# Kernel optimization log

Hardware: AMD Instinct MI355X
Metric: run time of the kernel (lower is better)

The kernel has to match this reference:

```python
import jax, jax.numpy as jnp
import numpy as np

IN_DIM, OUT_DIM, RANK = 4096, 4096, 16

def setup_inputs() -> dict:
    key = jax.random.key(0)
    k_x, k_w, k_a, k_b = jax.random.split(key, 4)
    x = jax.random.normal(k_x, (8, 2048, IN_DIM), dtype=jnp.float32)
    weight = jax.random.normal(k_w, (OUT_DIM, IN_DIM), dtype=jnp.float32)
    bias = jnp.zeros((OUT_DIM,), dtype=jnp.float32)
    # orthogonal-ish init for A, B via QR on gaussian
    A = jnp.linalg.qr(jax.random.normal(k_a, (IN_DIM, RANK), dtype=jnp.float32))[0]
    B = jnp.linalg.qr(jax.random.normal(k_b, (OUT_DIM, RANK), dtype=jnp.float32))[0].T
    return {"x": x, "A": A, "B": B, "weight": weight, "bias": bias}

def reference(x, A, B, weight, bias):
    # eval-mode dropout == identity, so
    # x @ (weight.T + A@B) + bias == x@weight.T + (x@A)@B + bias (fused low-rank path)
    base = jnp.einsum('bsd,od->bso', x, weight)
    lora = jnp.einsum('bsr,ro->bso', jnp.einsum('bsd,dr->bsr', x, A), B)
    return base + lora + bias
```

## Files before the change

### kernel.cpp

```cpp
#include <hip/hip_runtime.h>
#include <hip/hip_bf16.h>
#include <cstdint>

#define M_DIM 16384
#define K_DIM 4096
#define N_DIM 4096
#define RANK  16

#define BM 128
#define BN 128
#define BK 64

typedef __bf16 bf16x8 __attribute__((ext_vector_type(8)));
typedef float  f32x4  __attribute__((ext_vector_type(4)));

__device__ __forceinline__ uint16_t f2bf(float f) {
    union { float f; uint32_t u; } v; v.f = f;
    uint32_t u = v.u;
    return (uint16_t)((u + 0x7FFFu + ((u >> 16) & 1u)) >> 16);
}

#define CVT_BLOCKS (M_DIM * K_DIM / (8 * 256))

__global__ void prep_kernel(const float* __restrict__ x, uint16_t* __restrict__ xb,
                            const float* __restrict__ W, const float* __restrict__ A,
                            const float* __restrict__ B, uint16_t* __restrict__ wb) {
    if (blockIdx.x < CVT_BLOCKS) {
        size_t g = (size_t)blockIdx.x * blockDim.x + threadIdx.x;
        const float4* xv = (const float4*)x;
        float4 a = xv[2 * g];
        float4 b = xv[2 * g + 1];
        union { uint4 u; uint16_t h[8]; } p;
        p.h[0] = f2bf(a.x); p.h[1] = f2bf(a.y); p.h[2] = f2bf(a.z); p.h[3] = f2bf(a.w);
        p.h[4] = f2bf(b.x); p.h[5] = f2bf(b.y); p.h[6] = f2bf(b.z); p.h[7] = f2bf(b.w);
        ((uint4*)xb)[g] = p.u;
    } else {
        const int n = blockIdx.x - CVT_BLOCKS;
        __shared__ float bcol[RANK];
        if (threadIdx.x < RANK) bcol[threadIdx.x] = B[threadIdx.x * N_DIM + n];
        __syncthreads();
        float bc[RANK];
#pragma unroll
        for (int r = 0; r < RANK; r++) bc[r] = bcol[r];
        for (int k = threadIdx.x; k < K_DIM; k += blockDim.x) {
            const float4* ar = (const float4*)(A + (size_t)k * RANK);
            float acc = W[(size_t)n * K_DIM + k];
#pragma unroll
            for (int q = 0; q < 4; q++) {
                float4 a4 = ar[q];
                acc += a4.x * bc[4*q+0] + a4.y * bc[4*q+1] + a4.z * bc[4*q+2] + a4.w * bc[4*q+3];
            }
            wb[(size_t)n * K_DIM + k] = f2bf(acc);
        }
    }
}

__device__ __forceinline__ void gload_lds16(const void* g, void* l) {
    __builtin_amdgcn_global_load_lds(
        (const __attribute__((address_space(1))) void*)g,
        (__attribute__((address_space(3))) void*)l,
        16, 0, 0);
}

__global__ __launch_bounds__(256, 3)
void gemm_bt_bias(const uint16_t* __restrict__ Xb,
                  const uint16_t* __restrict__ Wb,
                  const float* __restrict__ bias,
                  float* __restrict__ C) {
    __shared__ uint16_t As[BM * BK];
    __shared__ uint16_t Bs[BN * BK];

    const int tid  = threadIdx.x;
    const int wave = tid >> 6;
    const int lane = tid & 63;

    const int bm = blockIdx.y * BM;
    const int bn = blockIdx.x * BN;

    const int wm = (wave >> 1) * 64;
    const int wn = (wave & 1) * 64;

    const uint16_t* xg[4];
    const uint16_t* wg[4];
    uint16_t* lA[4];
    uint16_t* lB[4];
#pragma unroll
    for (int s = 0; s < 4; s++) {
        const int c   = tid + 256 * s;
        const int row = c >> 3;
        const int ql  = c & 7;
        const int qg  = ql ^ (row & 7);
        xg[s] = Xb + (size_t)(bm + row) * K_DIM + qg * 8;
        wg[s] = Wb + (size_t)(bn + row) * K_DIM + qg * 8;
        lA[s] = As + c * 8;
        lB[s] = Bs + c * 8;
    }

    const int m15 = lane & 15;
    const int kq  = lane >> 4;

    int aoff[4][2], boff[4][2];
#pragma unroll
    for (int i = 0; i < 4; i++) {
        const int ra = wm + i * 16 + m15;
        const int rb = wn + i * 16 + m15;
#pragma unroll
        for (int h = 0; h < 2; h++) {
            const int kc = h * 4 + kq;
            aoff[i][h] = (ra * 8 + (kc ^ (ra & 7))) * 8;
            boff[i][h] = (rb * 8 + (kc ^ (rb & 7))) * 8;
        }
    }

    f32x4 acc[4][4];
    const f32x4 zero = {0.f, 0.f, 0.f, 0.f};
#pragma unroll
    for (int i = 0; i < 4; i++)
#pragma unroll
        for (int j = 0; j < 4; j++) acc[i][j] = zero;

    for (int k0 = 0; k0 < K_DIM; k0 += BK) {
#pragma unroll
        for (int s = 0; s < 4; s++) gload_lds16(xg[s] + k0, lA[s]);
#pragma unroll
        for (int s = 0; s < 4; s++) gload_lds16(wg[s] + k0, lB[s]);
        __syncthreads();

#pragma unroll
        for (int h = 0; h < 2; h++) {
            bf16x8 af[4], bfr[4];
#pragma unroll
            for (int i = 0; i < 4; i++) af[i]  = *(const bf16x8*)&As[aoff[i][h]];
#pragma unroll
            for (int j = 0; j < 4; j++) bfr[j] = *(const bf16x8*)&Bs[boff[j][h]];
#pragma unroll
            for (int i = 0; i < 4; i++)
#pragma unroll
                for (int j = 0; j < 4; j++)
                    acc[i][j] = __builtin_amdgcn_mfma_f32_16x16x32_bf16(af[i], bfr[j], acc[i][j], 0, 0, 0);
        }

        __syncthreads();
    }

#pragma unroll
    for (int j = 0; j < 4; j++) {
        const int col = bn + wn + j * 16 + m15;
        const float bv = bias[col];
#pragma unroll
        for (int i = 0; i < 4; i++) {
            const int row0 = bm + wm + i * 16 + kq * 4;
#pragma unroll
            for (int r = 0; r < 4; r++) {
                C[(size_t)(row0 + r) * N_DIM + col] = acc[i][j][r] + bv;
            }
        }
    }
}

extern "C" void kernel_launch(void* const* d_in, const int* in_sizes, int n_in,
                              void* d_out, int out_size, void* d_ws, size_t ws_size,
                              hipStream_t stream) {
    const float* x    = (const float*)d_in[0];
    const float* A    = (const float*)d_in[1];
    const float* B    = (const float*)d_in[2];
    const float* W    = (const float*)d_in[3];
    const float* bias = (const float*)d_in[4];
    float* out = (float*)d_out;

    uint16_t* Xb = (uint16_t*)d_ws;
    uint16_t* Wb = (uint16_t*)((char*)d_ws + (size_t)M_DIM * K_DIM * sizeof(uint16_t));

    prep_kernel<<<CVT_BLOCKS + N_DIM, 256, 0, stream>>>(x, Xb, W, A, B, Wb);

    dim3 grid(N_DIM / BN, M_DIM / BM);
    gemm_bt_bias<<<grid, 256, 0, stream>>>(Xb, Wb, bias, out);
}
```

Measured before the change: 1.029 ms.

## Triple-buffer LDS pipeline with 256x128 tiles, block swizzle, and split prep kernels

Moves the GEMM to 256x128 tiles with 512 threads and a three-stage LDS ring buffer. Global-to-LDS loads for tile T+2 are issued between the MFMA halves of tile T, with explicit vmcnt waits and one barrier per iteration in place of two. Adds a grouped block-index swizzle for L2 reuse and raises wave priority around the MFMA bursts. The prep work is split into a grid-stride conversion kernel and a separate weight-merge kernel. The costs are more LDS per block (96KB), fewer resident blocks per CU, and dependence on hand-counted waitcnt values being correct.

```diff
diff --git a/kernel.cpp b/kernel.cpp
--- a/kernel.cpp
+++ b/kernel.cpp
@@ -1,5 +1,4 @@
 #include <hip/hip_runtime.h>
-#include <hip/hip_bf16.h>
 #include <cstdint>
 
 #define M_DIM 16384
@@ -7,9 +6,15 @@
 #define N_DIM 4096
 #define RANK  16
 
-#define BM 128
+#define BM 256
 #define BN 128
 #define BK 64
+#define NT (K_DIM / BK)
+
+#define A_ELEMS (BM * BK)
+#define B_ELEMS (BN * BK)
+#define BUF_ELEMS (A_ELEMS + B_ELEMS)
+#define LDS_ELEMS (3 * BUF_ELEMS)
 
 typedef __bf16 bf16x8 __attribute__((ext_vector_type(8)));
 typedef float  f32x4  __attribute__((ext_vector_type(4)));
@@ -20,13 +25,12 @@
     return (uint16_t)((u + 0x7FFFu + ((u >> 16) & 1u)) >> 16);
 }
 
-#define CVT_BLOCKS (M_DIM * K_DIM / (8 * 256))
-
-__global__ void prep_kernel(const float* __restrict__ x, uint16_t* __restrict__ xb,
-                            const float* __restrict__ W, const float* __restrict__ A,
-                            const float* __restrict__ B, uint16_t* __restrict__ wb) {
-    if (blockIdx.x < CVT_BLOCKS) {
-        size_t g = (size_t)blockIdx.x * blockDim.x + threadIdx.x;
+#define CVT_GRID 2048
+#define CVT_ITems (M_DIM * K_DIM / 8)
+
+__global__ void cvt_kernel(const float* __restrict__ x, uint16_t* __restrict__ xb) {
+    const size_t stride = (size_t)CVT_GRID * 256;
+    for (size_t g = (size_t)blockIdx.x * 256 + threadIdx.x; g < (size_t)CVT_ITems; g += stride) {
         const float4* xv = (const float4*)x;
         float4 a = xv[2 * g];
         float4 b = xv[2 * g + 1];
@@ -34,24 +38,27 @@
         p.h[0] = f2bf(a.x); p.h[1] = f2bf(a.y); p.h[2] = f2bf(a.z); p.h[3] = f2bf(a.w);
         p.h[4] = f2bf(b.x); p.h[5] = f2bf(b.y); p.h[6] = f2bf(b.z); p.h[7] = f2bf(b.w);
         ((uint4*)xb)[g] = p.u;
-    } else {
-        const int n = blockIdx.x - CVT_BLOCKS;
-        __shared__ float bcol[RANK];
-        if (threadIdx.x < RANK) bcol[threadIdx.x] = B[threadIdx.x * N_DIM + n];
-        __syncthreads();
-        float bc[RANK];
-#pragma unroll
-        for (int r = 0; r < RANK; r++) bc[r] = bcol[r];
-        for (int k = threadIdx.x; k < K_DIM; k += blockDim.x) {
-            const float4* ar = (const float4*)(A + (size_t)k * RANK);
-            float acc = W[(size_t)n * K_DIM + k];
-#pragma unroll
-            for (int q = 0; q < 4; q++) {
-                float4 a4 = ar[q];
-                acc += a4.x * bc[4*q+0] + a4.y * bc[4*q+1] + a4.z * bc[4*q+2] + a4.w * bc[4*q+3];
-            }
-            wb[(size_t)n * K_DIM + k] = f2bf(acc);
-        }
+    }
+}
+
+__global__ void weff_kernel(const float* __restrict__ W, const float* __restrict__ A,
+                            const float* __restrict__ B, uint16_t* __restrict__ wb) {
+    const int n = blockIdx.x;
+    __shared__ float bcol[RANK];
+    if (threadIdx.x < RANK) bcol[threadIdx.x] = B[threadIdx.x * N_DIM + n];
+    __syncthreads();
+    float bc[RANK];
+#pragma unroll
+    for (int r = 0; r < RANK; r++) bc[r] = bcol[r];
+    for (int k = threadIdx.x; k < K_DIM; k += 256) {
+        const float4* ar = (const float4*)(A + (size_t)k * RANK);
+        float acc = W[(size_t)n * K_DIM + k];
+#pragma unroll
+        for (int q = 0; q < 4; q++) {
+            float4 a4 = ar[q];
+            acc += a4.x * bc[4*q+0] + a4.y * bc[4*q+1] + a4.z * bc[4*q+2] + a4.w * bc[4*q+3];
+        }
+        wb[(size_t)n * K_DIM + k] = f2bf(acc);
     }
 }
 
@@ -62,53 +69,53 @@
         16, 0, 0);
 }
 
-__global__ __launch_bounds__(256, 3)
+__global__ __launch_bounds__(512, 2)
 void gemm_bt_bias(const uint16_t* __restrict__ Xb,
                   const uint16_t* __restrict__ Wb,
                   const float* __restrict__ bias,
                   float* __restrict__ C) {
-    __shared__ uint16_t As[BM * BK];
-    __shared__ uint16_t Bs[BN * BK];
+    __shared__ uint16_t smem[LDS_ELEMS];
 
     const int tid  = threadIdx.x;
     const int wave = tid >> 6;
     const int lane = tid & 63;
-
-    const int bm = blockIdx.y * BM;
-    const int bn = blockIdx.x * BN;
-
-    const int wm = (wave >> 1) * 64;
-    const int wn = (wave & 1) * 64;
-
-    const uint16_t* xg[4];
-    const uint16_t* wg[4];
-    uint16_t* lA[4];
-    uint16_t* lB[4];
-#pragma unroll
-    for (int s = 0; s < 4; s++) {
-        const int c   = tid + 256 * s;
-        const int row = c >> 3;
-        const int ql  = c & 7;
-        const int qg  = ql ^ (row & 7);
-        xg[s] = Xb + (size_t)(bm + row) * K_DIM + qg * 8;
-        wg[s] = Wb + (size_t)(bn + row) * K_DIM + qg * 8;
-        lA[s] = As + c * 8;
-        lB[s] = Bs + c * 8;
-    }
-
+    const int wm = wave >> 1;
+    const int wn = wave & 1;
     const int m15 = lane & 15;
     const int kq  = lane >> 4;
 
+    const int lin = blockIdx.y * gridDim.x + blockIdx.x;
+    const int swz = (lin & 7) * (2048 / 8) + (lin >> 3);
+    const int bn = (swz & 31) * BN;
+    const int bm = (swz >> 5) * BM;
+
+    const uint16_t* aSrc[4]; int aDst[4];
+    const uint16_t* bSrc[2]; int bDst[2];
+#pragma unroll
+    for (int s = 0; s < 4; s++) {
+        const int c = tid + 512 * s;
+        const int row = c >> 3, qg = (c & 7) ^ (row & 7);
+        aSrc[s] = Xb + (size_t)(bm + row) * K_DIM + qg * 8;
+        aDst[s] = c * 8;
+    }
+#pragma unroll
+    for (int s = 0; s < 2; s++) {
+        const int c = tid + 512 * s;
+        const int row = c >> 3, qg = (c & 7) ^ (row & 7);
+        bSrc[s] = Wb + (size_t)(bn + row) * K_DIM + qg * 8;
+        bDst[s] = A_ELEMS + c * 8;
+    }
+
     int aoff[4][2], boff[4][2];
 #pragma unroll
     for (int i = 0; i < 4; i++) {
-        const int ra = wm + i * 16 + m15;
-        const int rb = wn + i * 16 + m15;
+        const int ra = wm * 64 + i * 16 + m15;
+        const int rb = wn * 64 + i * 16 + m15;
 #pragma unroll
         for (int h = 0; h < 2; h++) {
             const int kc = h * 4 + kq;
-            aoff[i][h] = (ra * 8 + (kc ^ (ra & 7))) * 8;
-            boff[i][h] = (rb * 8 + (kc ^ (rb & 7))) * 8;
+            aoff[i][h] = ra * BK + (kc ^ (ra & 7)) * 8;
+            boff[i][h] = A_ELEMS + rb * BK + (kc ^ (rb & 7)) * 8;
         }
     }
 
@@ -119,37 +126,83 @@
 #pragma unroll
         for (int j = 0; j < 4; j++) acc[i][j] = zero;
 
-    for (int k0 = 0; k0 < K_DIM; k0 += BK) {
-#pragma unroll
-        for (int s = 0; s < 4; s++) gload_lds16(xg[s] + k0, lA[s]);
-#pragma unroll
-        for (int s = 0; s < 4; s++) gload_lds16(wg[s] + k0, lB[s]);
-        __syncthreads();
-
-#pragma unroll
-        for (int h = 0; h < 2; h++) {
+#pragma unroll
+    for (int s = 0; s < 4; s++) gload_lds16(aSrc[s], &smem[aDst[s]]);
+#pragma unroll
+    for (int s = 0; s < 2; s++) gload_lds16(bSrc[s], &smem[bDst[s]]);
+#pragma unroll
+    for (int s = 0; s < 4; s++) gload_lds16(aSrc[s] + BK, &smem[BUF_ELEMS + aDst[s]]);
+#pragma unroll
+    for (int s = 0; s < 2; s++) gload_lds16(bSrc[s] + BK, &smem[BUF_ELEMS + bDst[s]]);
+    asm volatile("s_waitcnt vmcnt(6) lgkmcnt(0)" ::: "memory");
+    __builtin_amdgcn_s_barrier();
+    __builtin_amdgcn_sched_barrier(0);
+
+    int rbO = 0;
+    int sbO = 2 * BUF_ELEMS;
+
+#pragma unroll 1
+    for (int T = 0; T < NT; ++T) {
+        const bool st = (T + 2 < NT);
+        const int kst = (T + 2) * BK;
+
+        if (st) {
+            gload_lds16(aSrc[0] + kst, &smem[sbO + aDst[0]]);
+            gload_lds16(aSrc[1] + kst, &smem[sbO + aDst[1]]);
+            gload_lds16(bSrc[0] + kst, &smem[sbO + bDst[0]]);
+        }
+        {
             bf16x8 af[4], bfr[4];
 #pragma unroll
-            for (int i = 0; i < 4; i++) af[i]  = *(const bf16x8*)&As[aoff[i][h]];
-#pragma unroll
-            for (int j = 0; j < 4; j++) bfr[j] = *(const bf16x8*)&Bs[boff[j][h]];
+            for (int i = 0; i < 4; i++) af[i]  = *(const bf16x8*)&smem[rbO + aoff[i][0]];
+#pragma unroll
+            for (int j = 0; j < 4; j++) bfr[j] = *(const bf16x8*)&smem[rbO + boff[j][0]];
+            __builtin_amdgcn_s_setprio(1);
 #pragma unroll
             for (int i = 0; i < 4; i++)
 #pragma unroll
                 for (int j = 0; j < 4; j++)
                     acc[i][j] = __builtin_amdgcn_mfma_f32_16x16x32_bf16(af[i], bfr[j], acc[i][j], 0, 0, 0);
-        }
-
-        __syncthreads();
+            __builtin_amdgcn_s_setprio(0);
+        }
+
+        if (st) {
+            gload_lds16(aSrc[2] + kst, &smem[sbO + aDst[2]]);
+            gload_lds16(aSrc[3] + kst, &smem[sbO + aDst[3]]);
+            gload_lds16(bSrc[1] + kst, &smem[sbO + bDst[1]]);
+        }
+        {
+            bf16x8 af[4], bfr[4];
+#pragma unroll
+            for (int i = 0; i < 4; i++) af[i]  = *(const bf16x8*)&smem[rbO + aoff[i][1]];
+#pragma unroll
+            for (int j = 0; j < 4; j++) bfr[j] = *(const bf16x8*)&smem[rbO + boff[j][1]];
+            __builtin_amdgcn_s_setprio(1);
+#pragma unroll
+            for (int i = 0; i < 4; i++)
+#pragma unroll
+                for (int j = 0; j < 4; j++)
+                    acc[i][j] = __builtin_amdgcn_mfma_f32_16x16x32_bf16(af[i], bfr[j], acc[i][j], 0, 0, 0);
+            __builtin_amdgcn_s_setprio(0);
+        }
+
+        if (T < NT - 1) {
+            if (st) asm volatile("s_waitcnt vmcnt(6) lgkmcnt(0)" ::: "memory");
+            else    asm volatile("s_waitcnt vmcnt(0) lgkmcnt(0)" ::: "memory");
+            __builtin_amdgcn_s_barrier();
+            __builtin_amdgcn_sched_barrier(0);
+        }
+        rbO += BUF_ELEMS; if (rbO == LDS_ELEMS) rbO = 0;
+        sbO += BUF_ELEMS; if (sbO == LDS_ELEMS) sbO = 0;
     }
 
 #pragma unroll
     for (int j = 0; j < 4; j++) {
-        const int col = bn + wn + j * 16 + m15;
+        const int col = bn + wn * 64 + j * 16 + m15;
         const float bv = bias[col];
 #pragma unroll
         for (int i = 0; i < 4; i++) {
-            const int row0 = bm + wm + i * 16 + kq * 4;
+            const int row0 = bm + wm * 64 + i * 16 + kq * 4;
 #pragma unroll
             for (int r = 0; r < 4; r++) {
                 C[(size_t)(row0 + r) * N_DIM + col] = acc[i][j][r] + bv;
@@ -171,8 +224,9 @@
     uint16_t* Xb = (uint16_t*)d_ws;
     uint16_t* Wb = (uint16_t*)((char*)d_ws + (size_t)M_DIM * K_DIM * sizeof(uint16_t));
 
-    prep_kernel<<<CVT_BLOCKS + N_DIM, 256, 0, stream>>>(x, Xb, W, A, B, Wb);
+    cvt_kernel<<<CVT_GRID, 256, 0, stream>>>(x, Xb);
+    weff_kernel<<<N_DIM, 256, 0, stream>>>(W, A, B, Wb);
 
     dim3 grid(N_DIM / BN, M_DIM / BM);
-    gemm_bt_bias<<<grid, 256, 0, stream>>>(Xb, Wb, bias, out);
-}
+    gemm_bt_bias<<<grid, 512, 0, stream>>>(Xb, Wb, bias, out);
+}
```

Result: slower. 1.089 ms (+5.9%).

## Use 256x256 tiles with double-buffered async LDS loads and phased MFMA schedule

Applied to the files above, without the earlier changes.

Rewrites the bf16 GEMM to use 256x256 block tiles with 512 threads (8 waves, each covering 128x64). LDS is double-buffered and global-to-LDS loads are issued two k-steps ahead. The MFMA work is split into four sub-phases interleaved with fragment reads, barriers and setprio. A grid swizzle is added for L2 locality. The aim is to hide global memory latency, raise arithmetic intensity and reduce per-tile barrier stalls, at the cost of 128KB of LDS, more registers and lower occupancy.

```diff
diff --git a/kernel.cpp b/kernel.cpp
--- a/kernel.cpp
+++ b/kernel.cpp
@@ -1,5 +1,4 @@
 #include <hip/hip_runtime.h>
-#include <hip/hip_bf16.h>
 #include <cstdint>
 
 #define M_DIM 16384
@@ -7,9 +6,15 @@
 #define N_DIM 4096
 #define RANK  16
 
-#define BM 128
-#define BN 128
+#define BM 256
+#define BN 256
 #define BK 64
+#define NT (K_DIM / BK)
+
+#define HALF_ELEMS 8192
+#define TILE_ELEMS (2 * HALF_ELEMS)
+#define LDS_ELEMS  (4 * TILE_ELEMS)
+#define B_BYTE_BASE 65536
 
 typedef __bf16 bf16x8 __attribute__((ext_vector_type(8)));
 typedef float  f32x4  __attribute__((ext_vector_type(4)));
@@ -55,101 +60,177 @@
     }
 }
 
-__device__ __forceinline__ void gload_lds16(const void* g, void* l) {
-    __builtin_amdgcn_global_load_lds(
-        (const __attribute__((address_space(1))) void*)g,
-        (__attribute__((address_space(3))) void*)l,
-        16, 0, 0);
-}
-
-__global__ __launch_bounds__(256, 3)
+#define GL(g, l) __builtin_amdgcn_global_load_lds( \
+    (const __attribute__((address_space(1))) void*)(g), \
+    (__attribute__((address_space(3))) void*)(l), 16, 0, 0)
+
+#define MFMA1(d, a, b) (d) = __builtin_amdgcn_mfma_f32_16x16x32_bf16((a), (b), (d), 0, 0, 0)
+
+#define BAR() asm volatile("s_barrier" ::: "memory")
+
+__global__ __launch_bounds__(512, 2)
 void gemm_bt_bias(const uint16_t* __restrict__ Xb,
                   const uint16_t* __restrict__ Wb,
                   const float* __restrict__ bias,
                   float* __restrict__ C) {
-    __shared__ uint16_t As[BM * BK];
-    __shared__ uint16_t Bs[BN * BK];
+    __shared__ uint16_t smem[LDS_ELEMS];
 
     const int tid  = threadIdx.x;
     const int wave = tid >> 6;
     const int lane = tid & 63;
-
-    const int bm = blockIdx.y * BM;
-    const int bn = blockIdx.x * BN;
-
-    const int wm = (wave >> 1) * 64;
-    const int wn = (wave & 1) * 64;
-
-    const uint16_t* xg[4];
-    const uint16_t* wg[4];
-    uint16_t* lA[4];
-    uint16_t* lB[4];
-#pragma unroll
-    for (int s = 0; s < 4; s++) {
-        const int c   = tid + 256 * s;
-        const int row = c >> 3;
-        const int ql  = c & 7;
-        const int qg  = ql ^ (row & 7);
-        xg[s] = Xb + (size_t)(bm + row) * K_DIM + qg * 8;
-        wg[s] = Wb + (size_t)(bn + row) * K_DIM + qg * 8;
-        lA[s] = As + c * 8;
-        lB[s] = Bs + c * 8;
-    }
-
+    const int wm  = wave >> 2;
+    const int wn  = wave & 3;
     const int m15 = lane & 15;
     const int kq  = lane >> 4;
-
-    int aoff[4][2], boff[4][2];
-#pragma unroll
-    for (int i = 0; i < 4; i++) {
-        const int ra = wm + i * 16 + m15;
-        const int rb = wn + i * 16 + m15;
-#pragma unroll
-        for (int h = 0; h < 2; h++) {
-            const int kc = h * 4 + kq;
-            aoff[i][h] = (ra * 8 + (kc ^ (ra & 7))) * 8;
-            boff[i][h] = (rb * 8 + (kc ^ (rb & 7))) * 8;
+    const int r7  = m15 & 7;
+
+    const int lin = blockIdx.y * gridDim.x + blockIdx.x;
+    const int swz = (lin & 7) * 128 + (lin >> 3);
+    const int bn = (swz & 15) * BN;
+    const int bm = (swz >> 4) * BM;
+
+    const int c0 = tid, c1 = tid + 512;
+    const int sr0 = c0 >> 3, sr1 = c1 >> 3;
+    const int sq0 = (c0 & 7) ^ (sr0 & 7), sq1 = (c1 & 7) ^ (sr1 & 7);
+    const uint16_t* aS0 = Xb + (size_t)(bm + sr0) * K_DIM + sq0 * 8;
+    const uint16_t* aS1 = Xb + (size_t)(bm + sr1) * K_DIM + sq1 * 8;
+    const uint16_t* bS0 = Wb + (size_t)(bn + sr0) * K_DIM + sq0 * 8;
+    const uint16_t* bS1 = Wb + (size_t)(bn + sr1) * K_DIM + sq1 * 8;
+    const int dE0 = c0 * 8, dE1 = c1 * 8;
+    const size_t hOF = (size_t)128 * K_DIM;
+
+#define STAGE_A(bufe, kcol) do { \
+        GL(aS0 + (kcol),       &smem[(bufe) + dE0]); \
+        GL(aS1 + (kcol),       &smem[(bufe) + dE1]); \
+        GL(aS0 + hOF + (kcol), &smem[(bufe) + HALF_ELEMS + dE0]); \
+        GL(aS1 + hOF + (kcol), &smem[(bufe) + HALF_ELEMS + dE1]); \
+    } while (0)
+#define STAGE_B(bufe, kcol) do { \
+        GL(bS0 + (kcol),       &smem[2 * TILE_ELEMS + (bufe) + dE0]); \
+        GL(bS1 + (kcol),       &smem[2 * TILE_ELEMS + (bufe) + dE1]); \
+        GL(bS0 + hOF + (kcol), &smem[2 * TILE_ELEMS + (bufe) + HALF_ELEMS + dE0]); \
+        GL(bS1 + hOF + (kcol), &smem[2 * TILE_ELEMS + (bufe) + HALF_ELEMS + dE1]); \
+    } while (0)
+
+    const int aoff0 = m15 * 128 + ((kq ^ r7) << 4);
+    const int aoff1 = aoff0 ^ 64;
+    const int boff0 = ((wn & 1) * 64 + m15) * 128 + ((kq ^ r7) << 4);
+    const int boff1 = boff0 ^ 64;
+
+    f32x4 acc[8][4];
+    const f32x4 zero = {0.f, 0.f, 0.f, 0.f};
+#pragma unroll
+    for (int i = 0; i < 8; i++)
+#pragma unroll
+        for (int j = 0; j < 4; j++) acc[i][j] = zero;
+
+    STAGE_A(0, 0); STAGE_B(0, 0);
+    STAGE_A(TILE_ELEMS, BK); STAGE_B(TILE_ELEMS, BK);
+    asm volatile("s_waitcnt vmcnt(8)" ::: "memory");
+    BAR();
+    __builtin_amdgcn_sched_barrier(0);
+
+    const char* sbase = (const char*)smem;
+
+#pragma unroll 1
+    for (int T = 0; T < NT; ++T) {
+        const int bufe = (T & 1) * TILE_ELEMS;
+        const bool st = (T + 2 < NT);
+        const int kst = (T + 2) * BK;
+
+        const char* pA = sbase + (T & 1) * 32768 + wm * 16384;
+        const char* pB = sbase + B_BYTE_BASE + (T & 1) * 32768 + (wn >> 1) * 16384;
+
+        bf16x8 aF[4][2], bF[4][2];
+
+#pragma unroll
+        for (int i = 0; i < 4; i++) {
+            aF[i][0] = *(const bf16x8*)(pA + i * 2048 + aoff0);
+            aF[i][1] = *(const bf16x8*)(pA + i * 2048 + aoff1);
+        }
+#pragma unroll
+        for (int j = 0; j < 2; j++) {
+            bF[j][0] = *(const bf16x8*)(pB + j * 2048 + boff0);
+            bF[j][1] = *(const bf16x8*)(pB + j * 2048 + boff1);
+        }
+        BAR();
+        asm volatile("s_waitcnt lgkmcnt(0)" ::: "memory");
+        __builtin_amdgcn_sched_barrier(0);
+        __builtin_amdgcn_s_setprio(1);
+#pragma unroll
+        for (int i = 0; i < 4; i++)
+#pragma unroll
+            for (int j = 0; j < 2; j++) {
+                MFMA1(acc[i][j], aF[i][0], bF[j][0]);
+                MFMA1(acc[i][j], aF[i][1], bF[j][1]);
+            }
+        __builtin_amdgcn_s_setprio(0);
+        BAR();
+
+#pragma unroll
+        for (int j = 2; j < 4; j++) {
+            bF[j][0] = *(const bf16x8*)(pB + j * 2048 + boff0);
+            bF[j][1] = *(const bf16x8*)(pB + j * 2048 + boff1);
+        }
+        BAR();
+        asm volatile("s_waitcnt lgkmcnt(0)" ::: "memory");
+        __builtin_amdgcn_sched_barrier(0);
+        __builtin_amdgcn_s_setprio(1);
+#pragma unroll
+        for (int i = 0; i < 4; i++)
+#pragma unroll
+            for (int j = 0; j < 2; j++) {
+                MFMA1(acc[i][2 + j], aF[i][0], bF[2 + j][0]);
+                MFMA1(acc[i][2 + j], aF[i][1], bF[2 + j][1]);
+            }
+        __builtin_amdgcn_s_setprio(0);
+        BAR();
+
+#pragma unroll
+        for (int i = 0; i < 4; i++) {
+            aF[i][0] = *(const bf16x8*)(pA + (4 + i) * 2048 + aoff0);
+            aF[i][1] = *(const bf16x8*)(pA + (4 + i) * 2048 + aoff1);
+        }
+        if (st) STAGE_B(bufe, kst);
+        BAR();
+        asm volatile("s_waitcnt lgkmcnt(0)" ::: "memory");
+        __builtin_amdgcn_sched_barrier(0);
+        __builtin_amdgcn_s_setprio(1);
+#pragma unroll
+        for (int i = 0; i < 4; i++)
+#pragma unroll
+            for (int j = 0; j < 2; j++) {
+                MFMA1(acc[4 + i][2 + j], aF[i][0], bF[2 + j][0]);
+                MFMA1(acc[4 + i][2 + j], aF[i][1], bF[2 + j][1]);
+            }
+        __builtin_amdgcn_s_setprio(0);
+        BAR();
+
+        if (st) STAGE_A(bufe, kst);
+        __builtin_amdgcn_s_setprio(1);
+#pragma unroll
+        for (int i = 0; i < 4; i++)
+#pragma unroll
+            for (int j = 0; j < 2; j++) {
+                MFMA1(acc[4 + i][j], aF[i][0], bF[j][0]);
+                MFMA1(acc[4 + i][j], aF[i][1], bF[j][1]);
+            }
+        __builtin_amdgcn_s_setprio(0);
+        if (T < NT - 1) {
+            if (st) asm volatile("s_waitcnt vmcnt(8)" ::: "memory");
+            else    asm volatile("s_waitcnt vmcnt(0)" ::: "memory");
+            BAR();
+            __builtin_amdgcn_sched_barrier(0);
         }
     }
 
-    f32x4 acc[4][4];
-    const f32x4 zero = {0.f, 0.f, 0.f, 0.f};
-#pragma unroll
-    for (int i = 0; i < 4; i++)
-#pragma unroll
-        for (int j = 0; j < 4; j++) acc[i][j] = zero;
-
-    for (int k0 = 0; k0 < K_DIM; k0 += BK) {
-#pragma unroll
-        for (int s = 0; s < 4; s++) gload_lds16(xg[s] + k0, lA[s]);
-#pragma unroll
-        for (int s = 0; s < 4; s++) gload_lds16(wg[s] + k0, lB[s]);
-        __syncthreads();
-
-#pragma unroll
-        for (int h = 0; h < 2; h++) {
-            bf16x8 af[4], bfr[4];
-#pragma unroll
-            for (int i = 0; i < 4; i++) af[i]  = *(const bf16x8*)&As[aoff[i][h]];
-#pragma unroll
-            for (int j = 0; j < 4; j++) bfr[j] = *(const bf16x8*)&Bs[boff[j][h]];
-#pragma unroll
-            for (int i = 0; i < 4; i++)
-#pragma unroll
-                for (int j = 0; j < 4; j++)
-                    acc[i][j] = __builtin_amdgcn_mfma_f32_16x16x32_bf16(af[i], bfr[j], acc[i][j], 0, 0, 0);
-        }
-
-        __syncthreads();
-    }
-
 #pragma unroll
     for (int j = 0; j < 4; j++) {
-        const int col = bn + wn + j * 16 + m15;
+        const int col = bn + wn * 64 + j * 16 + m15;
         const float bv = bias[col];
 #pragma unroll
-        for (int i = 0; i < 4; i++) {
-            const int row0 = bm + wm + i * 16 + kq * 4;
+        for (int i = 0; i < 8; i++) {
+            const int row0 = bm + wm * 128 + i * 16 + kq * 4;
 #pragma unroll
             for (int r = 0; r < 4; r++) {
                 C[(size_t)(row0 + r) * N_DIM + col] = acc[i][j][r] + bv;
@@ -174,5 +255,5 @@
     prep_kernel<<<CVT_BLOCKS + N_DIM, 256, 0, stream>>>(x, Xb, W, A, B, Wb);
 
     dim3 grid(N_DIM / BN, M_DIM / BM);
-    gemm_bt_bias<<<grid, 256, 0, stream>>>(Xb, Wb, bias, out);
-}
+    gemm_bt_bias<<<grid, 512, 0, stream>>>(Xb, Wb, bias, out);
+}
```

After: 982.3 us. 1.05x faster.
